# Performance work log

Measured on AMD Instinct MI355X. Metric: run time of the kernel, lower is better.

Reference implementation:

```python
import jax, jax.numpy as jnp
import numpy as np
import math

DIM = 1024
N_HEADS = 16
HEAD_DIM = DIM // N_HEADS
MAX_SEQ_LEN = 2048


def rope_tables(seq_len, head_dim):
    inv_freq = 1.0 / (10000.0 ** (jnp.arange(0, head_dim, 2, dtype=jnp.float32) / head_dim))
    t = jnp.arange(seq_len, dtype=jnp.float32)
    freqs = jnp.einsum('i,j->ij', t, inv_freq)          # [T, D/2]
    emb = jnp.concatenate([freqs, freqs], axis=-1)      # [T, D]
    return jnp.cos(emb), jnp.sin(emb)


def rotate_half(x):
    x1, x2 = jnp.split(x, 2, axis=-1)
    return jnp.concatenate([-x2, x1], axis=-1)


def setup_inputs() -> dict:
    key = jax.random.key(0)
    k1, k2, k3 = jax.random.split(key, 3)
    B, T = 4, 2048
    x = jax.random.normal(k1, (B, T, DIM), dtype=jnp.float32)
    # Linear(dim, 3*dim, bias=False) and Linear(dim, dim, bias=False); stored as [in, out]
    Wqkv = jax.random.normal(k2, (DIM, 3 * DIM), dtype=jnp.float32) * (1.0 / math.sqrt(DIM))
    Wproj = jax.random.normal(k3, (DIM, DIM), dtype=jnp.float32) * (1.0 / math.sqrt(DIM))
    return {"x": x, "Wqkv": Wqkv, "Wproj": Wproj}


def reference(x, Wqkv, Wproj):
    B, T, C = x.shape
    qkv = x @ Wqkv                                       # [B,T,3C]
    q, k, v = jnp.split(qkv, 3, axis=-1)
    # [B,T,C] -> [B,H,T,D]
    def to_heads(t_):
        return t_.reshape(B, T, N_HEADS, HEAD_DIM).transpose(0, 2, 1, 3)
    q, k, v = to_heads(q), to_heads(k), to_heads(v)
    cos, sin = rope_tables(T, HEAD_DIM)                  # [T,D]
    cos = cos[None, None, :, :]
    sin = sin[None, None, :, :]
    q = q * cos + rotate_half(q) * sin
    k = k * cos + rotate_half(k) * sin
    scale = 1.0 / math.sqrt(HEAD_DIM)
    att = jnp.einsum('bhqd,bhkd->bhqk', q, k) * scale    # [B,H,T,T]
    causal = jnp.triu(jnp.ones((T, T), dtype=bool), k=1)
    att = jnp.where(causal[None, None], -jnp.inf, att)
    att = jax.nn.softmax(att, axis=-1)
    y = jnp.einsum('bhqk,bhkd->bhqd', att, v)            # [B,H,T,D]
    y = y.transpose(0, 2, 1, 3).reshape(B, T, C)
    return y @ Wproj
```

## Files before the change

### kernel.cpp

```cpp
#include <hip/hip_runtime.h>
#include <hip/hip_bf16.h>

typedef unsigned short u16;
typedef __attribute__((ext_vector_type(8))) short short8;
typedef __attribute__((ext_vector_type(4))) float floatx4;

__device__ __forceinline__ u16 f2bf(float f) {
    union { float f; unsigned u; } v; v.f = f;
    unsigned r = v.u + 0x7fffu + ((v.u >> 16) & 1u);
    return (u16)(r >> 16);
}
__device__ __forceinline__ float fexp2(float x) {
#if __has_builtin(__builtin_amdgcn_exp2f)
    return __builtin_amdgcn_exp2f(x);
#else
    return exp2f(x);
#endif
}
__device__ __forceinline__ unsigned cvtpk_bf16(float lo, float hi) {
    unsigned r;
    asm("v_cvt_pk_bf16_f32 %0, %1, %2" : "=v"(r) : "v"(lo), "v"(hi));
    return r;
}
__device__ __forceinline__ void permlane32_swap(unsigned &a, unsigned &b) {
    asm("v_permlane32_swap_b32 %0, %1" : "+v"(a), "+v"(b));
}
__device__ __forceinline__ void permlane16_swap(unsigned &a, unsigned &b) {
    asm("v_permlane16_swap_b32 %0, %1" : "+v"(a), "+v"(b));
}

__device__ __forceinline__ void async_load16(const void* g, void* l) {
    __builtin_amdgcn_global_load_lds(
        (const __attribute__((address_space(1))) unsigned int*)g,
        (__attribute__((address_space(3))) unsigned int*)l, 16, 0, 0);
}

#define B_   4
#define T_   2048
#define NH_  16
#define HD_  64
#define DIM_ 1024
#define M_   (B_ * T_)
#define NQKV (3 * DIM_)
#define NT_  16
#define LOG2E 1.4426950408889634f

__global__ __launch_bounds__(256) void preproc(const float* __restrict__ x,
                                               const float* __restrict__ Wqkv,
                                               const float* __restrict__ Wproj,
                                               u16* __restrict__ xb,
                                               u16* __restrict__ wqt,
                                               u16* __restrict__ wpt,
                                               float* __restrict__ tabc,
                                               float* __restrict__ tabs) {
    __shared__ float tile[32][33];
    const int bid = blockIdx.x, tid = threadIdx.x;
    if (bid < 8192) {
        int idx = bid * 256 + tid;
        float4 v = ((const float4*)x)[idx];
        ushort4 o;
        o.x = f2bf(v.x); o.y = f2bf(v.y); o.z = f2bf(v.z); o.w = f2bf(v.w);
        ((ushort4*)xb)[idx] = o;
    } else if (bid < 12288) {
        const float* in; u16* outp; int Cn, bx, by;
        if (bid < 11264) { int blk = bid - 8192;  in = Wqkv;  outp = wqt; Cn = NQKV; bx = blk % 96; by = blk / 96; }
        else             { int blk = bid - 11264; in = Wproj; outp = wpt; Cn = DIM_; bx = blk & 31; by = blk >> 5; }
        const int R = DIM_;
        int c0 = bx * 32, r0 = by * 32;
        int tx = tid & 31, ty = tid >> 5;
#pragma unroll
        for (int i = 0; i < 4; ++i)
            tile[ty + i * 8][tx] = in[(size_t)(r0 + ty + i * 8) * Cn + c0 + tx];
        __syncthreads();
#pragma unroll
        for (int i = 0; i < 4; ++i)
            outp[(size_t)(c0 + ty + i * 8) * R + r0 + tx] = f2bf(tile[tx][ty + i * 8]);
    } else {
        int idx = (bid - 12288) * 256 + tid;
        int t = idx >> 5, j = idx & 31;
        double invf = pow(10000.0, -(double)j / 32.0);
        double th = (double)t * invf;
        tabc[idx] = (float)cos(th);
        tabs[idx] = (float)sin(th);
    }
}

__device__ __forceinline__ void gemm_core(const u16* __restrict__ A,
                                          const u16* __restrict__ Bt,
                                          u16* smem, int m0, int n0, int tid,
                                          floatx4 (&acc)[4][4]) {
    const int wave = tid >> 6, lane = tid & 63;
    const int ln15 = lane & 15, quad = lane >> 4;
    const int wm = (wave & 1) * 64, wn = (wave >> 1) * 64;
    const int l8 = lane & 7, ld8 = lane >> 3;
    const int sgc = (l8 ^ ld8) * 8;
    const int K = DIM_;

    const u16* aS = A + (size_t)(m0 + wave * 16 + ld8) * K + sgc;
    const u16* bS = Bt + (size_t)(n0 + wave * 32 + ld8) * K + sgc;

    auto issueA_B0 = [&](int k2, u16* As2, u16* Bs2) {
        async_load16(aS + k2,          As2 + (wave * 16) * 64);
        async_load16(aS + 8 * K + k2,  As2 + (wave * 16 + 8) * 64);
        async_load16(bS + k2,          Bs2 + (wave * 32) * 64);
    };
    auto issueB123 = [&](int k2, u16* Bs2) {
        async_load16(bS + 8 * K + k2,  Bs2 + (wave * 32 + 8) * 64);
        async_load16(bS + 16 * K + k2, Bs2 + (wave * 32 + 16) * 64);
        async_load16(bS + 24 * K + k2, Bs2 + (wave * 32 + 24) * 64);
    };
    auto compute = [&](const u16* As_c, const u16* Bs_c, int c4) {
        short8 af[4], bfv[4];
#pragma unroll
        for (int i = 0; i < 4; ++i) {
            int row = wm + i * 16 + ln15;
            af[i] = *(const short8*)&As_c[row * 64 + (((c4 + quad) ^ (row & 7)) << 3)];
        }
#pragma unroll
        for (int j = 0; j < 4; ++j) {
            int row = wn + j * 16 + ln15;
            bfv[j] = *(const short8*)&Bs_c[row * 64 + (((c4 + quad) ^ (row & 7)) << 3)];
        }
        __builtin_amdgcn_s_setprio(1);
#pragma unroll
        for (int i = 0; i < 4; ++i)
#pragma unroll
            for (int j = 0; j < 4; ++j)
                acc[i][j] = __builtin_amdgcn_mfma_f32_16x16x32_bf16(
                    af[i], bfv[j], acc[i][j], 0, 0, 0);
        __builtin_amdgcn_s_setprio(0);
    };

    issueA_B0(0, smem, smem + 24576);
    issueB123(0, smem + 24576);
    issueA_B0(64, smem + 8192, smem + 24576 + 16384);
    issueB123(64, smem + 24576 + 16384);

#pragma unroll 1
    for (int t = 0; t < NT_; ++t) {
        if (t < NT_ - 1) asm volatile("s_waitcnt vmcnt(6)" ::: "memory");
        else             asm volatile("s_waitcnt vmcnt(0)" ::: "memory");
        __builtin_amdgcn_s_barrier();
        asm volatile("" ::: "memory");

        const int cb = t % 3, cb2 = (t + 2) % 3;
        const u16* As_c = smem + cb * 8192;
        const u16* Bs_c = smem + 24576 + cb * 16384;
        u16* As2 = smem + cb2 * 8192;
        u16* Bs2 = smem + 24576 + cb2 * 16384;
        const bool iss = t < NT_ - 2;
        const int k2 = (t + 2) * 64;

        if (iss) issueA_B0(k2, As2, Bs2);
        compute(As_c, Bs_c, 0);
        asm volatile("" ::: "memory");
        __builtin_amdgcn_s_barrier();
        asm volatile("" ::: "memory");

        if (iss) issueB123(k2, Bs2);
        compute(As_c, Bs_c, 4);
        asm volatile("" ::: "memory");
    }
}

__global__ __launch_bounds__(512, 2) void gemm_qkv(const u16* __restrict__ A,
                                                   const u16* __restrict__ Bt,
                                                   const float* __restrict__ tabc,
                                                   const float* __restrict__ tabs,
                                                   u16* __restrict__ Qo,
                                                   u16* __restrict__ Ko,
                                                   u16* __restrict__ Vt) {
    __shared__ __align__(16) u16 smem[73728];
    const int tid = threadIdx.x;
    const int bid = blockIdx.x;
    const int wg = (bid & 7) * 96 + (bid >> 3);
    const int bx = wg / 64, by = wg - bx * 64;
    const int m0 = by * 128, n0 = bx * 256;

    floatx4 acc[4][4] = {};
    gemm_core(A, Bt, smem, m0, n0, tid, acc);

    const int wave = tid >> 6, lane = tid & 63;
    const int ln15 = lane & 15, quad = lane >> 4;
    const int wm = (wave & 1) * 64, wn = (wave >> 1) * 64;

    __syncthreads();
    u16* Es = smem;
    const int sel = n0 >> 10;
    auto es_put = [&](int row, int col, u16 v) {
        int c = col >> 3;
        int pc = (c & 24) | ((c & 7) ^ (row & 7));
        Es[row * 256 + pc * 8 + (col & 7)] = v;
    };
    if (sel == 2) {
#pragma unroll
        for (int i = 0; i < 4; ++i)
#pragma unroll
            for (int j = 0; j < 4; ++j)
#pragma unroll
                for (int r = 0; r < 4; ++r)
                    es_put(wm + i * 16 + quad * 4 + r, wn + j * 16 + ln15,
                           f2bf(acc[i][j][r]));
    } else {
        const float scale = sel ? 1.0f : 0.125f * LOG2E;
#pragma unroll
        for (int i = 0; i < 4; ++i)
#pragma unroll
            for (int jjl = 0; jjl < 2; ++jjl) {
                int j = jjl * 16 + ln15;
#pragma unroll
                for (int r = 0; r < 4; ++r) {
                    int row = wm + i * 16 + quad * 4 + r;
                    int t = (m0 + row) & (T_ - 1);
                    float cs = tabc[t * 32 + j], sn = tabs[t * 32 + j];
                    float xl = acc[i][jjl][r], xh = acc[i][jjl + 2][r];
                    es_put(row, wn + j,      f2bf((xl * cs - xh * sn) * scale));
                    es_put(row, wn + j + 32, f2bf((xh * cs + xl * sn) * scale));
                }
            }
    }
    __syncthreads();
    if (sel == 2) {
        const int bq = m0 >> 11;
        const int t0 = m0 & (T_ - 1);
        const int h0 = (n0 & 1023) >> 6;
#pragma unroll
        for (int a = 0; a < 4; ++a) {
            int aid = tid + a * 512;
            int hh = aid >> 9;
            int rem = aid & 511;
            int tseg = rem >> 5;
            int d2 = rem & 31;
            int col = hh * 64 + 2 * d2;
            int cch = col >> 3;
            u16 lo8[8], hi8[8];
#pragma unroll
            for (int j = 0; j < 8; ++j) {
                int row = tseg * 8 + j;
                int pc = (cch & 24) | ((cch & 7) ^ (row & 7));
                unsigned w = *(const unsigned*)&Es[row * 256 + pc * 8 + (col & 7)];
                lo8[j] = (u16)(w & 0xffffu);
                hi8[j] = (u16)(w >> 16);
            }
            size_t ob = ((size_t)((bq * NH_ + h0 + hh) * HD_) + 2 * d2) * T_ + t0 + tseg * 8;
            *(uint4*)(Vt + ob) = *(const uint4*)lo8;
            *(uint4*)(Vt + ob + T_) = *(const uint4*)hi8;
        }
    } else {
        const int bb = m0 >> 11;
        u16* outqk = (sel == 1) ? Ko : Qo;
#pragma unroll
        for (int k = 0; k < 8; ++k) {
            int cid = tid + k * 512;
            int row = cid >> 5, c = cid & 31;
            int pc = (c & 24) | ((c & 7) ^ (row & 7));
            uint4 v = *(const uint4*)&Es[row * 256 + pc * 8];
            int h = ((n0 & 1023) >> 6) + (c >> 3);
            int d = (c & 7) * 8;
            int t = (m0 + row) & (T_ - 1);
            *(uint4*)&outqk[((size_t)(bb * NH_ + h) * T_ + t) * HD_ + d] = v;
        }
    }
}

__device__ __forceinline__ void gemm_core128(const u16* __restrict__ A,
                                             const u16* __restrict__ Bt,
                                             u16* smem, int m0, int n0, int tid,
                                             floatx4 (&acc)[4][4]) {
    const int wave = tid >> 6, lane = tid & 63;
    const int ln15 = lane & 15, quad = lane >> 4;
    const int wm = (wave & 1) * 64, wn = (wave >> 1) * 64;
    const int l8 = lane & 7, ld8 = lane >> 3;
    const int sgc = (l8 ^ ld8) * 8;
    const int K = DIM_;

    const u16* aS = A + (size_t)(m0 + wave * 32 + ld8) * K + sgc;
    const u16* bS = Bt + (size_t)(n0 + wave * 32 + ld8) * K + sgc;

    auto stage = [&](int k0, u16* buf) {
#pragma unroll
        for (int it = 0; it < 4; ++it) {
            async_load16(aS + (size_t)(it * 8) * K + k0,
                         buf + (wave * 32 + it * 8) * 64);
            async_load16(bS + (size_t)(it * 8) * K + k0,
                         buf + 8192 + (wave * 32 + it * 8) * 64);
        }
    };
    auto compute = [&](const u16* buf, int c4) {
        short8 af[4], bfv[4];
#pragma unroll
        for (int i = 0; i < 4; ++i) {
            int row = wm + i * 16 + ln15;
            af[i] = *(const short8*)&buf[row * 64 + (((c4 + quad) ^ (row & 7)) << 3)];
        }
#pragma unroll
        for (int j = 0; j < 4; ++j) {
            int row = wn + j * 16 + ln15;
            bfv[j] = *(const short8*)&buf[8192 + row * 64 + (((c4 + quad) ^ (row & 7)) << 3)];
        }
        __builtin_amdgcn_s_setprio(1);
#pragma unroll
        for (int i = 0; i < 4; ++i)
#pragma unroll
            for (int j = 0; j < 4; ++j)
                acc[i][j] = __builtin_amdgcn_mfma_f32_16x16x32_bf16(
                    af[i], bfv[j], acc[i][j], 0, 0, 0);
        __builtin_amdgcn_s_setprio(0);
    };

    stage(0, smem);
#pragma unroll 1
    for (int t = 0; t < NT_; ++t) {
        asm volatile("s_waitcnt vmcnt(0)" ::: "memory");
        __builtin_amdgcn_s_barrier();
        asm volatile("" ::: "memory");
        if (t + 1 < NT_) stage((t + 1) * 64, smem + ((t + 1) & 1) * 16384);
        const u16* cur = smem + (t & 1) * 16384;
        compute(cur, 0);
        compute(cur, 4);
        asm volatile("" ::: "memory");
    }
}

__global__ __launch_bounds__(256, 4) void gemm_proj(const u16* __restrict__ A,
                                                    const u16* __restrict__ Bt,
                                                    float* __restrict__ C) {
    __shared__ __align__(16) u16 smem[32768];
    const int tid = threadIdx.x;
    const int bid = blockIdx.x;
    const int local = bid >> 3;
    const int by = (bid & 7) * 8 + (local & 7);
    const int bx = local >> 3;
    const int m0 = by * 128, n0 = bx * 128;

    floatx4 acc[4][4] = {};
    gemm_core128(A, Bt, smem, m0, n0, tid, acc);

    const int wave = tid >> 6, lane = tid & 63;
    const int ln15 = lane & 15, quad = lane >> 4;
    const int wm = (wave & 1) * 64, wn = (wave >> 1) * 64;
#pragma unroll
    for (int i = 0; i < 4; ++i)
#pragma unroll
        for (int jj = 0; jj < 4; ++jj)
#pragma unroll
            for (int r = 0; r < 4; ++r) {
                int m = m0 + wm + i * 16 + quad * 4 + r;
                int n = n0 + wn + jj * 16 + ln15;
                C[(size_t)m * DIM_ + n] = acc[i][jj][r];
            }
}

__global__ __launch_bounds__(256, 4) void attn_kernel(const u16* __restrict__ Q,
                                                      const u16* __restrict__ Kh,
                                                      const u16* __restrict__ Vt,
                                                      u16* __restrict__ Y) {
    __shared__ __align__(16) u16 Kl[2][64 * 64];
    __shared__ __align__(16) u16 Vl[2][64 * 64];
    const int tid = threadIdx.x, wave = tid >> 6, lane = tid & 63;
    const int ln15 = lane & 15, quad = lane >> 4;
    const int bid = blockIdx.x;
    const int wg = (bid & 7) * 64 + (bid >> 3);
    const int p = wg & 7;
    const int bh = wg >> 3;
    const int b = bh >> 4, h = bh & 15;
    const int l8 = lane & 7, ld8 = lane >> 3;
    const int sgc = l8 ^ ld8;

    const u16* kbase = Kh + (size_t)bh * T_ * HD_;
    const u16* vbase = Vt + (size_t)bh * HD_ * T_;
    const short8 ones = {0x3F80, 0x3F80, 0x3F80, 0x3F80,
                         0x3F80, 0x3F80, 0x3F80, 0x3F80};
    const int srow = wave * 16;

#pragma unroll
    for (int half = 0; half < 2; ++half) {
        const int tidx = half ? p : (15 - p);
        const int q0 = tidx * 128;
        const int base_row = q0 + wave * 32;

        const u16* qp0 = Q + ((size_t)bh * T_ + base_row + ln15) * HD_;
        const u16* qp1 = qp0 + 16 * HD_;
        short8 qf00 = *(const short8*)(qp0 + quad * 8);
        short8 qf01 = *(const short8*)(qp0 + 32 + quad * 8);
        short8 qf10 = *(const short8*)(qp1 + quad * 8);
        short8 qf11 = *(const short8*)(qp1 + 32 + quad * 8);

        floatx4 o0[5] = {}, o1[5] = {};

        __syncthreads();
#pragma unroll
        for (int it = 0; it < 2; ++it) {
            int r = srow + it * 8;
            async_load16(kbase + (size_t)(r + ld8) * HD_ + sgc * 8, &Kl[0][r * 64]);
            async_load16(vbase + (size_t)(r + ld8) * T_ + sgc * 8, &Vl[0][r * 64]);
        }

        const int NKT = 2 * tidx + 1;
        for (int kt = 0; kt <= NKT; ++kt) {
            const int cur = kt & 1;
            __syncthreads();
            if (kt < NKT) {
                const int kn = (kt + 1) * 64;
#pragma unroll
                for (int it = 0; it < 2; ++it) {
                    int r = srow + it * 8;
                    async_load16(kbase + (size_t)(kn + r + ld8) * HD_ + sgc * 8,
                                 &Kl[cur ^ 1][r * 64]);
                    async_load16(vbase + (size_t)(r + ld8) * T_ + kn + sgc * 8,
                                 &Vl[cur ^ 1][r * 64]);
                }
            }
            floatx4 s0[4] = {}, s1[4] = {};
            __builtin_amdgcn_s_setprio(1);
#pragma unroll
            for (int nt = 0; nt < 4; ++nt) {
                int row = nt * 16 + ln15;
                short8 kf0 = *(const short8*)&Kl[cur][row * 64 + ((quad ^ (row & 7)) << 3)];
                short8 kf1 = *(const short8*)&Kl[cur][row * 64 + (((4 + quad) ^ (row & 7)) << 3)];
                s0[nt] = __builtin_amdgcn_mfma_f32_16x16x32_bf16(kf0, qf00, s0[nt], 0, 0, 0);
                s0[nt] = __builtin_amdgcn_mfma_f32_16x16x32_bf16(kf1, qf01, s0[nt], 0, 0, 0);
                s1[nt] = __builtin_amdgcn_mfma_f32_16x16x32_bf16(kf0, qf10, s1[nt], 0, 0, 0);
                s1[nt] = __builtin_amdgcn_mfma_f32_16x16x32_bf16(kf1, qf11, s1[nt], 0, 0, 0);
            }
            __builtin_amdgcn_s_setprio(0);
            if (kt >= 2 * tidx) {
                const int koff = (kt - 2 * tidx) * 64;
                const int lim0 = wave * 32 + ln15;
#pragma unroll
                for (int nt = 0; nt < 4; ++nt) {
                    int key = koff + nt * 16 + quad * 4;
#pragma unroll
                    for (int r = 0; r < 4; ++r) {
                        s0[nt][r] = (key + r > lim0) ? 0.f : fexp2(s0[nt][r]);
                        s1[nt][r] = (key + r > lim0 + 16) ? 0.f : fexp2(s1[nt][r]);
                    }
                }
            } else {
#pragma unroll
                for (int nt = 0; nt < 4; ++nt)
#pragma unroll
                    for (int r = 0; r < 4; ++r) {
                        s0[nt][r] = fexp2(s0[nt][r]);
                        s1[nt][r] = fexp2(s1[nt][r]);
                    }
            }
            union { unsigned u[4]; short8 s8; } pa0, pb0, pa1, pb1;
            {
                unsigned x0 = cvtpk_bf16(s0[0][0], s0[0][1]);
                unsigned x1 = cvtpk_bf16(s0[1][0], s0[1][1]);
                unsigned y0 = cvtpk_bf16(s0[0][2], s0[0][3]);
                unsigned y1 = cvtpk_bf16(s0[1][2], s0[1][3]);
                unsigned x2 = cvtpk_bf16(s0[2][0], s0[2][1]);
                unsigned x3 = cvtpk_bf16(s0[3][0], s0[3][1]);
                unsigned y2 = cvtpk_bf16(s0[2][2], s0[2][3]);
                unsigned y3 = cvtpk_bf16(s0[3][2], s0[3][3]);
                permlane32_swap(x0, x1); permlane16_swap(x0, x1);
                permlane32_swap(y0, y1); permlane16_swap(y0, y1);
                permlane32_swap(x2, x3); permlane16_swap(x2, x3);
                permlane32_swap(y2, y3); permlane16_swap(y2, y3);
                pa0.u[0] = x0; pa0.u[1] = y0; pa0.u[2] = x1; pa0.u[3] = y1;
                pb0.u[0] = x2; pb0.u[1] = y2; pb0.u[2] = x3; pb0.u[3] = y3;
            }
            {
                unsigned x0 = cvtpk_bf16(s1[0][0], s1[0][1]);
                unsigned x1 = cvtpk_bf16(s1[1][0], s1[1][1]);
                unsigned y0 = cvtpk_bf16(s1[0][2], s1[0][3]);
                unsigned y1 = cvtpk_bf16(s1[1][2], s1[1][3]);
                unsigned x2 = cvtpk_bf16(s1[2][0], s1[2][1]);
                unsigned x3 = cvtpk_bf16(s1[3][0], s1[3][1]);
                unsigned y2 = cvtpk_bf16(s1[2][2], s1[2][3]);
                unsigned y3 = cvtpk_bf16(s1[3][2], s1[3][3]);
                permlane32_swap(x0, x1); permlane16_swap(x0, x1);
                permlane32_swap(y0, y1); permlane16_swap(y0, y1);
                permlane32_swap(x2, x3); permlane16_swap(x2, x3);
                permlane32_swap(y2, y3); permlane16_swap(y2, y3);
                pa1.u[0] = x0; pa1.u[1] = y0; pa1.u[2] = x1; pa1.u[3] = y1;
                pb1.u[0] = x2; pb1.u[1] = y2; pb1.u[2] = x3; pb1.u[3] = y3;
            }
            __builtin_amdgcn_s_setprio(1);
#pragma unroll
            for (int nt = 0; nt < 4; ++nt) {
                int row = nt * 16 + ln15;
                short8 vf0 = *(const short8*)&Vl[cur][row * 64 + ((quad ^ (row & 7)) << 3)];
                short8 vf1 = *(const short8*)&Vl[cur][row * 64 + (((4 + quad) ^ (row & 7)) << 3)];
                o0[nt] = __builtin_amdgcn_mfma_f32_16x16x32_bf16(pa0.s8, vf0, o0[nt], 0, 0, 0);
                o0[nt] = __builtin_amdgcn_mfma_f32_16x16x32_bf16(pb0.s8, vf1, o0[nt], 0, 0, 0);
                o1[nt] = __builtin_amdgcn_mfma_f32_16x16x32_bf16(pa1.s8, vf0, o1[nt], 0, 0, 0);
                o1[nt] = __builtin_amdgcn_mfma_f32_16x16x32_bf16(pb1.s8, vf1, o1[nt], 0, 0, 0);
            }
            o0[4] = __builtin_amdgcn_mfma_f32_16x16x32_bf16(pa0.s8, ones, o0[4], 0, 0, 0);
            o0[4] = __builtin_amdgcn_mfma_f32_16x16x32_bf16(pb0.s8, ones, o0[4], 0, 0, 0);
            o1[4] = __builtin_amdgcn_mfma_f32_16x16x32_bf16(pa1.s8, ones, o1[4], 0, 0, 0);
            o1[4] = __builtin_amdgcn_mfma_f32_16x16x32_bf16(pb1.s8, ones, o1[4], 0, 0, 0);
            __builtin_amdgcn_s_setprio(0);
        }
#pragma unroll
        for (int r = 0; r < 4; ++r) {
            float inv0 = 1.f / o0[4][r];
            int row0 = base_row + quad * 4 + r;
            u16* yp0 = Y + ((size_t)(b * T_ + row0)) * DIM_ + h * HD_;
#pragma unroll
            for (int nt = 0; nt < 4; ++nt)
                yp0[nt * 16 + ln15] = f2bf(o0[nt][r] * inv0);
            float inv1 = 1.f / o1[4][r];
            u16* yp1 = yp0 + (size_t)16 * DIM_;
#pragma unroll
            for (int nt = 0; nt < 4; ++nt)
                yp1[nt * 16 + ln15] = f2bf(o1[nt][r] * inv1);
        }
    }
}

extern "C" void kernel_launch(void* const* d_in, const int* in_sizes, int n_in,
                              void* d_out, int out_size, void* d_ws, size_t ws_size,
                              hipStream_t stream) {
    const float* x     = (const float*)d_in[0];
    const float* Wqkv  = (const float*)d_in[1];
    const float* Wproj = (const float*)d_in[2];
    float* out = (float*)d_out;
    char* ws = (char*)d_ws;

    const size_t SZ_XB  = (size_t)M_ * DIM_ * 2;
    const size_t SZ_WQT = (size_t)NQKV * DIM_ * 2;
    const size_t SZ_WPT = (size_t)DIM_ * DIM_ * 2;
    const size_t SZ_Q   = SZ_XB;
    const size_t SZ_TAB = (size_t)T_ * 32 * 4;

    u16*   xb   = (u16*)(ws);
    u16*   wqt  = (u16*)(ws + SZ_XB);
    u16*   wpt  = (u16*)(ws + SZ_XB + SZ_WQT);
    u16*   qb   = (u16*)(ws + SZ_XB + SZ_WQT + SZ_WPT);
    u16*   kb   = (u16*)(ws + SZ_XB + SZ_WQT + SZ_WPT + SZ_Q);
    u16*   vtb  = (u16*)(ws + SZ_XB + SZ_WQT + SZ_WPT + 3 * SZ_Q);
    float* tabc = (float*)(ws + SZ_XB + SZ_WQT + SZ_WPT + 4 * SZ_Q);
    float* tabs = (float*)(ws + SZ_XB + SZ_WQT + SZ_WPT + 4 * SZ_Q + SZ_TAB);
    u16*   yb   = xb;

    preproc<<<12544, 256, 0, stream>>>(x, Wqkv, Wproj, xb, wqt, wpt, tabc, tabs);
    gemm_qkv<<<768, 512, 0, stream>>>(xb, wqt, tabc, tabs, qb, kb, vtb);
    attn_kernel<<<512, 256, 0, stream>>>(qb, kb, vtb, yb);
    gemm_proj<<<512, 256, 0, stream>>>(yb, wpt, out);
}
```

Before: 245.7 us.

## Drop LDS staging in attention and read K/V directly from global memory

The attention kernel stops double-buffering K and V tiles through shared memory with async loads and barriers. Each wave now loads its K and V MFMA fragments straight from global memory, leaving L2/L1 caches to provide the reuse across the four waves. The paired light/heavy query-tile scheme (two tiles per block) becomes one tile per block on a 1024-block grid, ordered heaviest first. This removes barriers and LDS traffic but multiplies global/cache loads per block, adds latency with no explicit prefetch, and gives up the per-block load balancing.

```diff
diff --git a/kernel.cpp b/kernel.cpp
--- a/kernel.cpp
+++ b/kernel.cpp
@@ -355,160 +355,128 @@
                                                       const u16* __restrict__ Kh,
                                                       const u16* __restrict__ Vt,
                                                       u16* __restrict__ Y) {
-    __shared__ __align__(16) u16 Kl[2][64 * 64];
-    __shared__ __align__(16) u16 Vl[2][64 * 64];
     const int tid = threadIdx.x, wave = tid >> 6, lane = tid & 63;
     const int ln15 = lane & 15, quad = lane >> 4;
     const int bid = blockIdx.x;
-    const int wg = (bid & 7) * 64 + (bid >> 3);
-    const int p = wg & 7;
-    const int bh = wg >> 3;
+    const int tidx = 15 - (bid >> 6);
+    const int bh = bid & 63;
     const int b = bh >> 4, h = bh & 15;
-    const int l8 = lane & 7, ld8 = lane >> 3;
-    const int sgc = l8 ^ ld8;
 
     const u16* kbase = Kh + (size_t)bh * T_ * HD_;
     const u16* vbase = Vt + (size_t)bh * HD_ * T_;
     const short8 ones = {0x3F80, 0x3F80, 0x3F80, 0x3F80,
                          0x3F80, 0x3F80, 0x3F80, 0x3F80};
-    const int srow = wave * 16;
-
-#pragma unroll
-    for (int half = 0; half < 2; ++half) {
-        const int tidx = half ? p : (15 - p);
-        const int q0 = tidx * 128;
-        const int base_row = q0 + wave * 32;
-
-        const u16* qp0 = Q + ((size_t)bh * T_ + base_row + ln15) * HD_;
-        const u16* qp1 = qp0 + 16 * HD_;
-        short8 qf00 = *(const short8*)(qp0 + quad * 8);
-        short8 qf01 = *(const short8*)(qp0 + 32 + quad * 8);
-        short8 qf10 = *(const short8*)(qp1 + quad * 8);
-        short8 qf11 = *(const short8*)(qp1 + 32 + quad * 8);
-
-        floatx4 o0[5] = {}, o1[5] = {};
-
-        __syncthreads();
-#pragma unroll
-        for (int it = 0; it < 2; ++it) {
-            int r = srow + it * 8;
-            async_load16(kbase + (size_t)(r + ld8) * HD_ + sgc * 8, &Kl[0][r * 64]);
-            async_load16(vbase + (size_t)(r + ld8) * T_ + sgc * 8, &Vl[0][r * 64]);
-        }
-
-        const int NKT = 2 * tidx + 1;
-        for (int kt = 0; kt <= NKT; ++kt) {
-            const int cur = kt & 1;
-            __syncthreads();
-            if (kt < NKT) {
-                const int kn = (kt + 1) * 64;
-#pragma unroll
-                for (int it = 0; it < 2; ++it) {
-                    int r = srow + it * 8;
-                    async_load16(kbase + (size_t)(kn + r + ld8) * HD_ + sgc * 8,
-                                 &Kl[cur ^ 1][r * 64]);
-                    async_load16(vbase + (size_t)(r + ld8) * T_ + kn + sgc * 8,
-                                 &Vl[cur ^ 1][r * 64]);
+
+    const int base_row = tidx * 128 + wave * 32;
+
+    const u16* qp0 = Q + ((size_t)bh * T_ + base_row + ln15) * HD_;
+    const u16* qp1 = qp0 + 16 * HD_;
+    short8 qf00 = *(const short8*)(qp0 + quad * 8);
+    short8 qf01 = *(const short8*)(qp0 + 32 + quad * 8);
+    short8 qf10 = *(const short8*)(qp1 + quad * 8);
+    short8 qf11 = *(const short8*)(qp1 + 32 + quad * 8);
+
+    floatx4 o0[5] = {}, o1[5] = {};
+
+    const int NKT = 2 * tidx + 1;
+    for (int kt = 0; kt <= NKT; ++kt) {
+        floatx4 s0[4] = {}, s1[4] = {};
+        __builtin_amdgcn_s_setprio(1);
+#pragma unroll
+        for (int nt = 0; nt < 4; ++nt) {
+            const u16* kp = kbase + (size_t)(kt * 64 + nt * 16 + ln15) * HD_;
+            short8 kf0 = *(const short8*)(kp + quad * 8);
+            short8 kf1 = *(const short8*)(kp + 32 + quad * 8);
+            s0[nt] = __builtin_amdgcn_mfma_f32_16x16x32_bf16(kf0, qf00, s0[nt], 0, 0, 0);
+            s0[nt] = __builtin_amdgcn_mfma_f32_16x16x32_bf16(kf1, qf01, s0[nt], 0, 0, 0);
+            s1[nt] = __builtin_amdgcn_mfma_f32_16x16x32_bf16(kf0, qf10, s1[nt], 0, 0, 0);
+            s1[nt] = __builtin_amdgcn_mfma_f32_16x16x32_bf16(kf1, qf11, s1[nt], 0, 0, 0);
+        }
+        __builtin_amdgcn_s_setprio(0);
+        if (kt >= 2 * tidx) {
+            const int koff = (kt - 2 * tidx) * 64;
+            const int lim0 = wave * 32 + ln15;
+#pragma unroll
+            for (int nt = 0; nt < 4; ++nt) {
+                int key = koff + nt * 16 + quad * 4;
+#pragma unroll
+                for (int r = 0; r < 4; ++r) {
+                    s0[nt][r] = (key + r > lim0) ? 0.f : fexp2(s0[nt][r]);
+                    s1[nt][r] = (key + r > lim0 + 16) ? 0.f : fexp2(s1[nt][r]);
                 }
             }
-            floatx4 s0[4] = {}, s1[4] = {};
-            __builtin_amdgcn_s_setprio(1);
-#pragma unroll
-            for (int nt = 0; nt < 4; ++nt) {
-                int row = nt * 16 + ln15;
-                short8 kf0 = *(const short8*)&Kl[cur][row * 64 + ((quad ^ (row & 7)) << 3)];
-                short8 kf1 = *(const short8*)&Kl[cur][row * 64 + (((4 + quad) ^ (row & 7)) << 3)];
-                s0[nt] = __builtin_amdgcn_mfma_f32_16x16x32_bf16(kf0, qf00, s0[nt], 0, 0, 0);
-                s0[nt] = __builtin_amdgcn_mfma_f32_16x16x32_bf16(kf1, qf01, s0[nt], 0, 0, 0);
-                s1[nt] = __builtin_amdgcn_mfma_f32_16x16x32_bf16(kf0, qf10, s1[nt], 0, 0, 0);
-                s1[nt] = __builtin_amdgcn_mfma_f32_16x16x32_bf16(kf1, qf11, s1[nt], 0, 0, 0);
-            }
-            __builtin_amdgcn_s_setprio(0);
-            if (kt >= 2 * tidx) {
-                const int koff = (kt - 2 * tidx) * 64;
-                const int lim0 = wave * 32 + ln15;
-#pragma unroll
-                for (int nt = 0; nt < 4; ++nt) {
-                    int key = koff + nt * 16 + quad * 4;
-#pragma unroll
-                    for (int r = 0; r < 4; ++r) {
-                        s0[nt][r] = (key + r > lim0) ? 0.f : fexp2(s0[nt][r]);
-                        s1[nt][r] = (key + r > lim0 + 16) ? 0.f : fexp2(s1[nt][r]);
-                    }
+        } else {
+#pragma unroll
+            for (int nt = 0; nt < 4; ++nt)
+#pragma unroll
+                for (int r = 0; r < 4; ++r) {
+                    s0[nt][r] = fexp2(s0[nt][r]);
+                    s1[nt][r] = fexp2(s1[nt][r]);
                 }
-            } else {
-#pragma unroll
-                for (int nt = 0; nt < 4; ++nt)
-#pragma unroll
-                    for (int r = 0; r < 4; ++r) {
-                        s0[nt][r] = fexp2(s0[nt][r]);
-                        s1[nt][r] = fexp2(s1[nt][r]);
-                    }
-            }
-            union { unsigned u[4]; short8 s8; } pa0, pb0, pa1, pb1;
-            {
-                unsigned x0 = cvtpk_bf16(s0[0][0], s0[0][1]);
-                unsigned x1 = cvtpk_bf16(s0[1][0], s0[1][1]);
-                unsigned y0 = cvtpk_bf16(s0[0][2], s0[0][3]);
-                unsigned y1 = cvtpk_bf16(s0[1][2], s0[1][3]);
-                unsigned x2 = cvtpk_bf16(s0[2][0], s0[2][1]);
-                unsigned x3 = cvtpk_bf16(s0[3][0], s0[3][1]);
-                unsigned y2 = cvtpk_bf16(s0[2][2], s0[2][3]);
-                unsigned y3 = cvtpk_bf16(s0[3][2], s0[3][3]);
-                permlane32_swap(x0, x1); permlane16_swap(x0, x1);
-                permlane32_swap(y0, y1); permlane16_swap(y0, y1);
-                permlane32_swap(x2, x3); permlane16_swap(x2, x3);
-                permlane32_swap(y2, y3); permlane16_swap(y2, y3);
-                pa0.u[0] = x0; pa0.u[1] = y0; pa0.u[2] = x1; pa0.u[3] = y1;
-                pb0.u[0] = x2; pb0.u[1] = y2; pb0.u[2] = x3; pb0.u[3] = y3;
-            }
-            {
-                unsigned x0 = cvtpk_bf16(s1[0][0], s1[0][1]);
-                unsigned x1 = cvtpk_bf16(s1[1][0], s1[1][1]);
-                unsigned y0 = cvtpk_bf16(s1[0][2], s1[0][3]);
-                unsigned y1 = cvtpk_bf16(s1[1][2], s1[1][3]);
-                unsigned x2 = cvtpk_bf16(s1[2][0], s1[2][1]);
-                unsigned x3 = cvtpk_bf16(s1[3][0], s1[3][1]);
-                unsigned y2 = cvtpk_bf16(s1[2][2], s1[2][3]);
-                unsigned y3 = cvtpk_bf16(s1[3][2], s1[3][3]);
-                permlane32_swap(x0, x1); permlane16_swap(x0, x1);
-                permlane32_swap(y0, y1); permlane16_swap(y0, y1);
-                permlane32_swap(x2, x3); permlane16_swap(x2, x3);
-                permlane32_swap(y2, y3); permlane16_swap(y2, y3);
-                pa1.u[0] = x0; pa1.u[1] = y0; pa1.u[2] = x1; pa1.u[3] = y1;
-                pb1.u[0] = x2; pb1.u[1] = y2; pb1.u[2] = x3; pb1.u[3] = y3;
-            }
-            __builtin_amdgcn_s_setprio(1);
-#pragma unroll
-            for (int nt = 0; nt < 4; ++nt) {
-                int row = nt * 16 + ln15;
-                short8 vf0 = *(const short8*)&Vl[cur][row * 64 + ((quad ^ (row & 7)) << 3)];
-                short8 vf1 = *(const short8*)&Vl[cur][row * 64 + (((4 + quad) ^ (row & 7)) << 3)];
-                o0[nt] = __builtin_amdgcn_mfma_f32_16x16x32_bf16(pa0.s8, vf0, o0[nt], 0, 0, 0);
-                o0[nt] = __builtin_amdgcn_mfma_f32_16x16x32_bf16(pb0.s8, vf1, o0[nt], 0, 0, 0);
-                o1[nt] = __builtin_amdgcn_mfma_f32_16x16x32_bf16(pa1.s8, vf0, o1[nt], 0, 0, 0);
-                o1[nt] = __builtin_amdgcn_mfma_f32_16x16x32_bf16(pb1.s8, vf1, o1[nt], 0, 0, 0);
-            }
-            o0[4] = __builtin_amdgcn_mfma_f32_16x16x32_bf16(pa0.s8, ones, o0[4], 0, 0, 0);
-            o0[4] = __builtin_amdgcn_mfma_f32_16x16x32_bf16(pb0.s8, ones, o0[4], 0, 0, 0);
-            o1[4] = __builtin_amdgcn_mfma_f32_16x16x32_bf16(pa1.s8, ones, o1[4], 0, 0, 0);
-            o1[4] = __builtin_amdgcn_mfma_f32_16x16x32_bf16(pb1.s8, ones, o1[4], 0, 0, 0);
-            __builtin_amdgcn_s_setprio(0);
-        }
-#pragma unroll
-        for (int r = 0; r < 4; ++r) {
-            float inv0 = 1.f / o0[4][r];
-            int row0 = base_row + quad * 4 + r;
-            u16* yp0 = Y + ((size_t)(b * T_ + row0)) * DIM_ + h * HD_;
-#pragma unroll
-            for (int nt = 0; nt < 4; ++nt)
-                yp0[nt * 16 + ln15] = f2bf(o0[nt][r] * inv0);
-            float inv1 = 1.f / o1[4][r];
-            u16* yp1 = yp0 + (size_t)16 * DIM_;
-#pragma unroll
-            for (int nt = 0; nt < 4; ++nt)
-                yp1[nt * 16 + ln15] = f2bf(o1[nt][r] * inv1);
-        }
+        }
+        union { unsigned u[4]; short8 s8; } pa0, pb0, pa1, pb1;
+        {
+            unsigned x0 = cvtpk_bf16(s0[0][0], s0[0][1]);
+            unsigned x1 = cvtpk_bf16(s0[1][0], s0[1][1]);
+            unsigned y0 = cvtpk_bf16(s0[0][2], s0[0][3]);
+            unsigned y1 = cvtpk_bf16(s0[1][2], s0[1][3]);
+            unsigned x2 = cvtpk_bf16(s0[2][0], s0[2][1]);
+            unsigned x3 = cvtpk_bf16(s0[3][0], s0[3][1]);
+            unsigned y2 = cvtpk_bf16(s0[2][2], s0[2][3]);
+            unsigned y3 = cvtpk_bf16(s0[3][2], s0[3][3]);
+            permlane32_swap(x0, x1); permlane16_swap(x0, x1);
+            permlane32_swap(y0, y1); permlane16_swap(y0, y1);
+            permlane32_swap(x2, x3); permlane16_swap(x2, x3);
+            permlane32_swap(y2, y3); permlane16_swap(y2, y3);
+            pa0.u[0] = x0; pa0.u[1] = y0; pa0.u[2] = x1; pa0.u[3] = y1;
+            pb0.u[0] = x2; pb0.u[1] = y2; pb0.u[2] = x3; pb0.u[3] = y3;
+        }
+        {
+            unsigned x0 = cvtpk_bf16(s1[0][0], s1[0][1]);
+            unsigned x1 = cvtpk_bf16(s1[1][0], s1[1][1]);
+            unsigned y0 = cvtpk_bf16(s1[0][2], s1[0][3]);
+            unsigned y1 = cvtpk_bf16(s1[1][2], s1[1][3]);
+            unsigned x2 = cvtpk_bf16(s1[2][0], s1[2][1]);
+            unsigned x3 = cvtpk_bf16(s1[3][0], s1[3][1]);
+            unsigned y2 = cvtpk_bf16(s1[2][2], s1[2][3]);
+            unsigned y3 = cvtpk_bf16(s1[3][2], s1[3][3]);
+            permlane32_swap(x0, x1); permlane16_swap(x0, x1);
+            permlane32_swap(y0, y1); permlane16_swap(y0, y1);
+            permlane32_swap(x2, x3); permlane16_swap(x2, x3);
+            permlane32_swap(y2, y3); permlane16_swap(y2, y3);
+            pa1.u[0] = x0; pa1.u[1] = y0; pa1.u[2] = x1; pa1.u[3] = y1;
+            pb1.u[0] = x2; pb1.u[1] = y2; pb1.u[2] = x3; pb1.u[3] = y3;
+        }
+        __builtin_amdgcn_s_setprio(1);
+#pragma unroll
+        for (int nt = 0; nt < 4; ++nt) {
+            const u16* vp = vbase + (size_t)(nt * 16 + ln15) * T_ + kt * 64;
+            short8 vf0 = *(const short8*)(vp + quad * 8);
+            short8 vf1 = *(const short8*)(vp + 32 + quad * 8);
+            o0[nt] = __builtin_amdgcn_mfma_f32_16x16x32_bf16(pa0.s8, vf0, o0[nt], 0, 0, 0);
+            o0[nt] = __builtin_amdgcn_mfma_f32_16x16x32_bf16(pb0.s8, vf1, o0[nt], 0, 0, 0);
+            o1[nt] = __builtin_amdgcn_mfma_f32_16x16x32_bf16(pa1.s8, vf0, o1[nt], 0, 0, 0);
+            o1[nt] = __builtin_amdgcn_mfma_f32_16x16x32_bf16(pb1.s8, vf1, o1[nt], 0, 0, 0);
+        }
+        o0[4] = __builtin_amdgcn_mfma_f32_16x16x32_bf16(pa0.s8, ones, o0[4], 0, 0, 0);
+        o0[4] = __builtin_amdgcn_mfma_f32_16x16x32_bf16(pb0.s8, ones, o0[4], 0, 0, 0);
+        o1[4] = __builtin_amdgcn_mfma_f32_16x16x32_bf16(pa1.s8, ones, o1[4], 0, 0, 0);
+        o1[4] = __builtin_amdgcn_mfma_f32_16x16x32_bf16(pb1.s8, ones, o1[4], 0, 0, 0);
+        __builtin_amdgcn_s_setprio(0);
+    }
+#pragma unroll
+    for (int r = 0; r < 4; ++r) {
+        float inv0 = 1.f / o0[4][r];
+        int row0 = base_row + quad * 4 + r;
+        u16* yp0 = Y + ((size_t)(b * T_ + row0)) * DIM_ + h * HD_;
+#pragma unroll
+        for (int nt = 0; nt < 4; ++nt)
+            yp0[nt * 16 + ln15] = f2bf(o0[nt][r] * inv0);
+        float inv1 = 1.f / o1[4][r];
+        u16* yp1 = yp0 + (size_t)16 * DIM_;
+#pragma unroll
+        for (int nt = 0; nt < 4; ++nt)
+            yp1[nt * 16 + ln15] = f2bf(o1[nt][r] * inv1);
     }
 }
 
@@ -539,6 +507,6 @@
 
     preproc<<<12544, 256, 0, stream>>>(x, Wqkv, Wproj, xb, wqt, wpt, tabc, tabs);
     gemm_qkv<<<768, 512, 0, stream>>>(xb, wqt, tabc, tabs, qb, kb, vtb);
-    attn_kernel<<<512, 256, 0, stream>>>(qb, kb, vtb, yb);
+    attn_kernel<<<1024, 256, 0, stream>>>(qb, kb, vtb, yb);
     gemm_proj<<<512, 256, 0, stream>>>(yb, wpt, out);
 }
```

Result: slower. 332.5 us (+35.3%).
